# Performance work log

Measured on AMD Instinct MI355X. Metric: run time of the kernel, lower is better.

## Reference

```python
import jax, jax.numpy as jnp
import numpy as np

ALPHA_U = 1.0 / 10.0   # dt/tauu
ALPHA_V = 1.0 / 150.0  # dt/tauv
M = 10.0

def setup_inputs() -> dict:
    key = jax.random.key(0)
    ks = jax.random.split(key, 6)
    B, D_in, H = 8192, 1024, 2048
    stdv = 1.0 / np.sqrt(H)
    return {
        "x": jax.random.normal(ks[0], (B, D_in), dtype=jnp.float32),
        "u": jax.random.normal(ks[1], (B, H), dtype=jnp.float32),
        "v": jax.random.normal(ks[2], (B, H), dtype=jnp.float32),
        "win": jax.random.uniform(ks[3], (H, D_in), dtype=jnp.float32, minval=-stdv, maxval=stdv),
        "wr": jax.random.uniform(ks[4], (H, H), dtype=jnp.float32, minval=-stdv, maxval=stdv),
        "bias": jax.random.uniform(ks[5], (H,), dtype=jnp.float32, minval=-stdv, maxval=stdv),
    }

def reference(x, u, v, win, wr, bias):
    # v update: leaky blend toward m*u, then relu
    v_new = jax.nn.relu((1.0 - ALPHA_V) * v + (ALPHA_V * M) * u)
    # u update: leaky blend with input + recurrent drive minus adapted v
    drive = jnp.einsum('bi,hi->bh', x, win) + jnp.einsum('bk,hk->bh', u, wr) + bias - v_new
    u_new = jax.nn.relu((1.0 - ALPHA_U) * u + ALPHA_U * drive)
    return (u_new, v_new)
```

## Files before the change

kernel.cpp:

```cpp
#include <hip/hip_runtime.h>
#include <hip/hip_bf16.h>
#include <stdint.h>

#define B_DIM 8192
#define D_IN  1024
#define H_DIM 2048
#define K_DIM (D_IN + H_DIM)

#define CV_CONST  (1.0f - 1.0f/150.0f)
#define CUV_CONST (10.0f/150.0f)
#define CU_CONST  0.9f
#define AU_CONST  0.1f

typedef __attribute__((ext_vector_type(8))) short short8;
typedef __attribute__((ext_vector_type(4))) float floatx4;

__device__ __forceinline__ unsigned short f2bf(float f) {
    union { float f; unsigned u; } x; x.f = f;
    unsigned r = x.u + 0x7fffu + ((x.u >> 16) & 1u);
    return (unsigned short)(r >> 16);
}

#define N4_X   ((B_DIM * D_IN)  / 4)
#define N4_U   ((B_DIM * H_DIM) / 4)
#define N4_WIN ((H_DIM * D_IN)  / 4)
#define N4_WR  ((H_DIM * H_DIM) / 4)
#define N4_TOT (N4_X + N4_U + N4_WIN + N4_WR)

__global__ __launch_bounds__(256)
void pack_all(const float4* __restrict__ x, const float4* __restrict__ u,
              const float4* __restrict__ win, const float4* __restrict__ wr,
              unsigned short* __restrict__ Abf, unsigned short* __restrict__ Wbf) {
    int i = blockIdx.x * 256 + threadIdx.x;
    const float4* src; unsigned short* dst; int shift, mask, coloff;
    if (i < N4_X)                    { src = x;   dst = Abf; shift = 10; mask = 1023; coloff = 0;    }
    else if (i < N4_X + N4_U)        { i -= N4_X; src = u;   dst = Abf; shift = 11; mask = 2047; coloff = D_IN; }
    else if (i < N4_X + N4_U + N4_WIN){ i -= N4_X + N4_U; src = win; dst = Wbf; shift = 10; mask = 1023; coloff = 0; }
    else                             { i -= N4_X + N4_U + N4_WIN; src = wr; dst = Wbf; shift = 11; mask = 2047; coloff = D_IN; }
    int idx = i << 2;
    int r = idx >> shift;
    int c = idx & mask;
    float4 f = src[i];
    ushort4 o;
    o.x = f2bf(f.x); o.y = f2bf(f.y); o.z = f2bf(f.z); o.w = f2bf(f.w);
    *(ushort4*)(dst + (size_t)r * K_DIM + coloff + c) = o;
}

#define GLOAD_LDS16(gp, lp)                                                          \
    __builtin_amdgcn_global_load_lds(                                                \
        (const __attribute__((address_space(1))) unsigned int*)(gp),                 \
        (__attribute__((address_space(3))) unsigned int*)(lp), 16, 0, 0)

#define VMCNT(n)  asm volatile("s_waitcnt vmcnt(" #n ")" ::: "memory")
#define LGKM0     asm volatile("s_waitcnt lgkmcnt(0)" ::: "memory")
#define SCHEDB    __builtin_amdgcn_sched_barrier(0)
#define BAR       __builtin_amdgcn_s_barrier()
#define PRIO1     __builtin_amdgcn_s_setprio(1)
#define PRIO0     __builtin_amdgcn_s_setprio(0)

#define NT (K_DIM / 64)

#define ALO 0
#define BLO 16384
#define BHI 32768
#define AHI 49152

#define ES_STRIDE 68
#define ES_REGION (16 * ES_STRIDE)

__global__ __launch_bounds__(512, 2)
void gemm_fused(const unsigned short* __restrict__ A,
                const unsigned short* __restrict__ Wc,
                const float* __restrict__ u_in,
                const float* __restrict__ v_in,
                const float* __restrict__ bias,
                float* __restrict__ out)
{
    __shared__ __align__(16) unsigned char smem[131072];

    const int tid  = threadIdx.x;
    const int wave = tid >> 6;
    const int lane = tid & 63;
    const int wrh  = wave >> 2;
    const int wc   = wave & 3;

    const int bid   = blockIdx.x;
    const int wid   = ((bid & 7) << 5) | (bid >> 3);
    const int tileM = (wid >> 3) << 8;
    const int tileN = (wid & 7)  << 8;

    const int frow = lane & 15;
    const int g    = lane >> 4;

    const unsigned short* Ag = A  + (size_t)(tileM + (wave >> 1) * 16 + frow) * K_DIM
                                  + (wave & 1) * 32 + g * 8;
    const unsigned short* Bg = Wc + (size_t)(tileN + (wave >> 2) * 64 + ((wave >> 1) & 1) * 16 + frow) * K_DIM
                                  + (wave & 1) * 32 + g * 8;
    const size_t R128 = (size_t)128 * K_DIM;
    const size_t R64  = (size_t) 64 * K_DIM;
    const size_t R32  = (size_t) 32 * K_DIM;

    const int w1024 = wave << 10;

    const int aRd = (wrh << 13) + (lane << 4);
    const int bRd = (wc  << 12) + (lane << 4);

    GLOAD_LDS16(Ag,               smem + ALO + w1024);
    GLOAD_LDS16(Ag + R128,        smem + ALO + 8192 + w1024);
    GLOAD_LDS16(Bg,               smem + BLO + w1024);
    GLOAD_LDS16(Bg + R128,        smem + BLO + 8192 + w1024);
    GLOAD_LDS16(Bg + R32,         smem + BHI + w1024);
    GLOAD_LDS16(Bg + R32 + R128,  smem + BHI + 8192 + w1024);
    GLOAD_LDS16(Ag + R64,         smem + AHI + w1024);
    GLOAD_LDS16(Ag + R64 + R128,  smem + AHI + 8192 + w1024);

    floatx4 acc[8][4] = {};
    short8 Alo[4][2], Ahi[4][2], Bl[2][2], Bh[2][2];

#define RD_A(cb, unit, i2s) (*(const short8*)(smem + (cb) + (unit) + aRd + (i2s) * 1024))
#define RD_B(cb, unit, j2s) (*(const short8*)(smem + (cb) + (unit) + bRd + (j2s) * 1024))

#pragma unroll 2
    for (int t = 0; t < NT - 1; ++t) {
        const int cb = (t & 1) << 16;
        const int nb = cb ^ 65536;
        const size_t kk = (size_t)(t + 1) * 64;

        GLOAD_LDS16(Ag + kk,              smem + nb + ALO + w1024);
        GLOAD_LDS16(Ag + kk + R128,       smem + nb + ALO + 8192 + w1024);
        GLOAD_LDS16(Bg + kk,              smem + nb + BLO + w1024);
        GLOAD_LDS16(Bg + kk + R128,       smem + nb + BLO + 8192 + w1024);
        GLOAD_LDS16(Bg + kk + R32,        smem + nb + BHI + w1024);
        GLOAD_LDS16(Bg + kk + R32 + R128, smem + nb + BHI + 8192 + w1024);
        GLOAD_LDS16(Ag + kk + R64,        smem + nb + AHI + w1024);
        GLOAD_LDS16(Ag + kk + R64 + R128, smem + nb + AHI + 8192 + w1024);

        VMCNT(8);
        BAR;
        SCHEDB;

#pragma unroll
        for (int i = 0; i < 4; ++i) { Alo[i][0] = RD_A(cb, ALO, i*2); Alo[i][1] = RD_A(cb, ALO, i*2+1); }
#pragma unroll
        for (int j = 0; j < 2; ++j) { Bl[j][0] = RD_B(cb, BLO, j*2); Bl[j][1] = RD_B(cb, BLO, j*2+1); }
#pragma unroll
        for (int j = 0; j < 2; ++j) { Bh[j][0] = RD_B(cb, BHI, j*2); Bh[j][1] = RD_B(cb, BHI, j*2+1); }
#pragma unroll
        for (int i = 0; i < 4; ++i) { Ahi[i][0] = RD_A(cb, AHI, i*2); Ahi[i][1] = RD_A(cb, AHI, i*2+1); }

        PRIO1;
#pragma unroll
        for (int i = 0; i < 4; ++i)
#pragma unroll
            for (int j = 0; j < 2; ++j) {
                acc[i][j] = __builtin_amdgcn_mfma_f32_16x16x32_bf16(Alo[i][0], Bl[j][0], acc[i][j], 0, 0, 0);
                acc[i][j] = __builtin_amdgcn_mfma_f32_16x16x32_bf16(Alo[i][1], Bl[j][1], acc[i][j], 0, 0, 0);
            }
#pragma unroll
        for (int i = 0; i < 4; ++i)
#pragma unroll
            for (int j = 0; j < 2; ++j) {
                acc[i][2+j] = __builtin_amdgcn_mfma_f32_16x16x32_bf16(Alo[i][0], Bh[j][0], acc[i][2+j], 0, 0, 0);
                acc[i][2+j] = __builtin_amdgcn_mfma_f32_16x16x32_bf16(Alo[i][1], Bh[j][1], acc[i][2+j], 0, 0, 0);
            }
#pragma unroll
        for (int i = 0; i < 4; ++i)
#pragma unroll
            for (int j = 0; j < 2; ++j) {
                acc[4+i][2+j] = __builtin_amdgcn_mfma_f32_16x16x32_bf16(Ahi[i][0], Bh[j][0], acc[4+i][2+j], 0, 0, 0);
                acc[4+i][2+j] = __builtin_amdgcn_mfma_f32_16x16x32_bf16(Ahi[i][1], Bh[j][1], acc[4+i][2+j], 0, 0, 0);
            }
#pragma unroll
        for (int i = 0; i < 4; ++i)
#pragma unroll
            for (int j = 0; j < 2; ++j) {
                acc[4+i][j] = __builtin_amdgcn_mfma_f32_16x16x32_bf16(Ahi[i][0], Bl[j][0], acc[4+i][j], 0, 0, 0);
                acc[4+i][j] = __builtin_amdgcn_mfma_f32_16x16x32_bf16(Ahi[i][1], Bl[j][1], acc[4+i][j], 0, 0, 0);
            }
        PRIO0;

        LGKM0;
        BAR;
    }

    {
        const int cb = ((NT - 1) & 1) << 16;
        VMCNT(0);
        BAR;
        SCHEDB;
#pragma unroll
        for (int i = 0; i < 4; ++i) { Alo[i][0] = RD_A(cb, ALO, i*2); Alo[i][1] = RD_A(cb, ALO, i*2+1); }
#pragma unroll
        for (int j = 0; j < 2; ++j) { Bl[j][0] = RD_B(cb, BLO, j*2); Bl[j][1] = RD_B(cb, BLO, j*2+1); }
#pragma unroll
        for (int j = 0; j < 2; ++j) { Bh[j][0] = RD_B(cb, BHI, j*2); Bh[j][1] = RD_B(cb, BHI, j*2+1); }
#pragma unroll
        for (int i = 0; i < 4; ++i) { Ahi[i][0] = RD_A(cb, AHI, i*2); Ahi[i][1] = RD_A(cb, AHI, i*2+1); }

        PRIO1;
#pragma unroll
        for (int i = 0; i < 4; ++i)
#pragma unroll
            for (int j = 0; j < 2; ++j) {
                acc[i][j]     = __builtin_amdgcn_mfma_f32_16x16x32_bf16(Alo[i][0], Bl[j][0], acc[i][j],     0, 0, 0);
                acc[i][j]     = __builtin_amdgcn_mfma_f32_16x16x32_bf16(Alo[i][1], Bl[j][1], acc[i][j],     0, 0, 0);
                acc[i][2+j]   = __builtin_amdgcn_mfma_f32_16x16x32_bf16(Alo[i][0], Bh[j][0], acc[i][2+j],   0, 0, 0);
                acc[i][2+j]   = __builtin_amdgcn_mfma_f32_16x16x32_bf16(Alo[i][1], Bh[j][1], acc[i][2+j],   0, 0, 0);
                acc[4+i][2+j] = __builtin_amdgcn_mfma_f32_16x16x32_bf16(Ahi[i][0], Bh[j][0], acc[4+i][2+j], 0, 0, 0);
                acc[4+i][2+j] = __builtin_amdgcn_mfma_f32_16x16x32_bf16(Ahi[i][1], Bh[j][1], acc[4+i][2+j], 0, 0, 0);
                acc[4+i][j]   = __builtin_amdgcn_mfma_f32_16x16x32_bf16(Ahi[i][0], Bl[j][0], acc[4+i][j],   0, 0, 0);
                acc[4+i][j]   = __builtin_amdgcn_mfma_f32_16x16x32_bf16(Ahi[i][1], Bl[j][1], acc[4+i][j],   0, 0, 0);
            }
        PRIO0;
    }

    __syncthreads();

    float* Esf = (float*)smem;
    const int q    = lane >> 4;
    const int c16  = lane & 15;
    const int colg = tileN + wc * 64 + c16 * 4;
    const float4 b4 = *(const float4*)&bias[colg];
    const size_t outV = (size_t)B_DIM * H_DIM;

#pragma unroll
    for (int i = 0; i < 8; ++i) {
        float* Es = Esf + (wave * 2 + (i & 1)) * ES_REGION;
#pragma unroll
        for (int j = 0; j < 4; ++j)
#pragma unroll
            for (int r = 0; r < 4; ++r)
                Es[(q * 4 + r) * ES_STRIDE + j * 16 + c16] = acc[i][j][r];
#pragma unroll
        for (int rg = 0; rg < 4; rg++) {
            const int rloc = rg * 4 + q;
            const float4 a4 = *(const float4*)&Es[rloc * ES_STRIDE + c16 * 4];
            const size_t idx = (size_t)(tileM + wrh * 128 + i * 16 + rloc) * H_DIM + colg;
            const float4 u4 = *(const float4*)&u_in[idx];
            const float4 v4 = *(const float4*)&v_in[idx];
            float4 vn, un;
            vn.x = fmaxf(CV_CONST * v4.x + CUV_CONST * u4.x, 0.0f);
            vn.y = fmaxf(CV_CONST * v4.y + CUV_CONST * u4.y, 0.0f);
            vn.z = fmaxf(CV_CONST * v4.z + CUV_CONST * u4.z, 0.0f);
            vn.w = fmaxf(CV_CONST * v4.w + CUV_CONST * u4.w, 0.0f);
            un.x = fmaxf(CU_CONST * u4.x + AU_CONST * (a4.x + b4.x - vn.x), 0.0f);
            un.y = fmaxf(CU_CONST * u4.y + AU_CONST * (a4.y + b4.y - vn.y), 0.0f);
            un.z = fmaxf(CU_CONST * u4.z + AU_CONST * (a4.z + b4.z - vn.z), 0.0f);
            un.w = fmaxf(CU_CONST * u4.w + AU_CONST * (a4.w + b4.w - vn.w), 0.0f);
            *(float4*)&out[idx]        = un;
            *(float4*)&out[outV + idx] = vn;
        }
    }
}

extern "C" void kernel_launch(void* const* d_in, const int* in_sizes, int n_in,
                              void* d_out, int out_size, void* d_ws, size_t ws_size,
                              hipStream_t stream) {
    const float* x    = (const float*)d_in[0];
    const float* u    = (const float*)d_in[1];
    const float* v    = (const float*)d_in[2];
    const float* win  = (const float*)d_in[3];
    const float* wr   = (const float*)d_in[4];
    const float* bias = (const float*)d_in[5];
    float* out = (float*)d_out;

    unsigned short* Abf = (unsigned short*)d_ws;
    unsigned short* Wbf = Abf + (size_t)B_DIM * K_DIM;

    pack_all<<<N4_TOT / 256, 256, 0, stream>>>(
        (const float4*)x, (const float4*)u, (const float4*)win, (const float4*)wr,
        Abf, Wbf);

    gemm_fused<<<256, 512, 0, stream>>>(Abf, Wbf, u, v, bias, out);
}
```

Before: 389.3 us.

## Load B operand directly from global into registers and split main loop into phases

Stops staging the weight (B) tile through shared memory: each wave loads its own B fragments straight from global memory into double-buffered registers, while only the A tile still goes through LDS via direct global-to-LDS loads. The K loop is restructured into four MFMA phases with staggered A loads (lo/hi halves issued at different points) and explicit vmcnt/barrier placement. This cuts LDS traffic and LDS reads for B and frees shared-memory capacity. In exchange it uses more registers, duplicates B global loads across the waves of a block, adds more barriers, and depends on hand-tuned vmcnt counts being correct.

```diff
diff --git a/kernel.cpp b/kernel.cpp
--- a/kernel.cpp
+++ b/kernel.cpp
@@ -53,6 +53,7 @@
 
 #define VMCNT(n)  asm volatile("s_waitcnt vmcnt(" #n ")" ::: "memory")
 #define LGKM0     asm volatile("s_waitcnt lgkmcnt(0)" ::: "memory")
+#define CPIN      asm volatile("" ::: "memory")
 #define SCHEDB    __builtin_amdgcn_sched_barrier(0)
 #define BAR       __builtin_amdgcn_s_barrier()
 #define PRIO1     __builtin_amdgcn_s_setprio(1)
@@ -61,8 +62,6 @@
 #define NT (K_DIM / 64)
 
 #define ALO 0
-#define BLO 16384
-#define BHI 32768
 #define AHI 49152
 
 #define ES_STRIDE 68
@@ -94,122 +93,141 @@
 
     const unsigned short* Ag = A  + (size_t)(tileM + (wave >> 1) * 16 + frow) * K_DIM
                                   + (wave & 1) * 32 + g * 8;
-    const unsigned short* Bg = Wc + (size_t)(tileN + (wave >> 2) * 64 + ((wave >> 1) & 1) * 16 + frow) * K_DIM
-                                  + (wave & 1) * 32 + g * 8;
     const size_t R128 = (size_t)128 * K_DIM;
     const size_t R64  = (size_t) 64 * K_DIM;
-    const size_t R32  = (size_t) 32 * K_DIM;
+
+    const unsigned short* Br = Wc + (size_t)(tileN + wc * 64 + frow) * K_DIM + g * 8;
 
     const int w1024 = wave << 10;
 
     const int aRd = (wrh << 13) + (lane << 4);
-    const int bRd = (wc  << 12) + (lane << 4);
-
-    GLOAD_LDS16(Ag,               smem + ALO + w1024);
-    GLOAD_LDS16(Ag + R128,        smem + ALO + 8192 + w1024);
-    GLOAD_LDS16(Bg,               smem + BLO + w1024);
-    GLOAD_LDS16(Bg + R128,        smem + BLO + 8192 + w1024);
-    GLOAD_LDS16(Bg + R32,         smem + BHI + w1024);
-    GLOAD_LDS16(Bg + R32 + R128,  smem + BHI + 8192 + w1024);
-    GLOAD_LDS16(Ag + R64,         smem + AHI + w1024);
-    GLOAD_LDS16(Ag + R64 + R128,  smem + AHI + 8192 + w1024);
 
     floatx4 acc[8][4] = {};
-    short8 Alo[4][2], Ahi[4][2], Bl[2][2], Bh[2][2];
+    short8 Ar[4][2];
+    short8 Bb0[8], Bb1[8];
 
 #define RD_A(cb, unit, i2s) (*(const short8*)(smem + (cb) + (unit) + aRd + (i2s) * 1024))
-#define RD_B(cb, unit, j2s) (*(const short8*)(smem + (cb) + (unit) + bRd + (j2s) * 1024))
-
-#pragma unroll 2
-    for (int t = 0; t < NT - 1; ++t) {
-        const int cb = (t & 1) << 16;
-        const int nb = cb ^ 65536;
-        const size_t kk = (size_t)(t + 1) * 64;
-
-        GLOAD_LDS16(Ag + kk,              smem + nb + ALO + w1024);
-        GLOAD_LDS16(Ag + kk + R128,       smem + nb + ALO + 8192 + w1024);
-        GLOAD_LDS16(Bg + kk,              smem + nb + BLO + w1024);
-        GLOAD_LDS16(Bg + kk + R128,       smem + nb + BLO + 8192 + w1024);
-        GLOAD_LDS16(Bg + kk + R32,        smem + nb + BHI + w1024);
-        GLOAD_LDS16(Bg + kk + R32 + R128, smem + nb + BHI + 8192 + w1024);
-        GLOAD_LDS16(Ag + kk + R64,        smem + nb + AHI + w1024);
-        GLOAD_LDS16(Ag + kk + R64 + R128, smem + nb + AHI + 8192 + w1024);
-
-        VMCNT(8);
-        BAR;
-        SCHEDB;
-
-#pragma unroll
-        for (int i = 0; i < 4; ++i) { Alo[i][0] = RD_A(cb, ALO, i*2); Alo[i][1] = RD_A(cb, ALO, i*2+1); }
-#pragma unroll
-        for (int j = 0; j < 2; ++j) { Bl[j][0] = RD_B(cb, BLO, j*2); Bl[j][1] = RD_B(cb, BLO, j*2+1); }
-#pragma unroll
-        for (int j = 0; j < 2; ++j) { Bh[j][0] = RD_B(cb, BHI, j*2); Bh[j][1] = RD_B(cb, BHI, j*2+1); }
-#pragma unroll
-        for (int i = 0; i < 4; ++i) { Ahi[i][0] = RD_A(cb, AHI, i*2); Ahi[i][1] = RD_A(cb, AHI, i*2+1); }
-
+
+    GLOAD_LDS16(Ag,        smem + ALO + w1024);
+    GLOAD_LDS16(Ag + R128, smem + ALO + 8192 + w1024);
+    CPIN;
+#pragma unroll
+    for (int j = 0; j < 4; ++j) {
+        Bb0[j*2+0] = *(const short8*)(Br + (size_t)j * 16 * K_DIM);
+        Bb0[j*2+1] = *(const short8*)(Br + (size_t)j * 16 * K_DIM + 32);
+    }
+    CPIN;
+    GLOAD_LDS16(Ag + R64,        smem + AHI + w1024);
+    GLOAD_LDS16(Ag + R64 + R128, smem + AHI + 8192 + w1024);
+    VMCNT(10);
+    BAR; SCHEDB;
+
+#define TILE_BODY(T, CB, NB, BCUR, BNXT)                                             \
+    {                                                                                \
+        const size_t kk = (size_t)((T) + 1) * 64;                                    \
+                   \
+        GLOAD_LDS16(Ag + kk,        smem + (NB) + ALO + w1024);                      \
+        GLOAD_LDS16(Ag + kk + R128, smem + (NB) + ALO + 8192 + w1024);               \
+        _Pragma("unroll")                                                            \
+        for (int i = 0; i < 4; ++i) {                                                \
+            Ar[i][0] = RD_A(CB, ALO, i*2); Ar[i][1] = RD_A(CB, ALO, i*2+1);          \
+        }                                                                            \
+        VMCNT(4); BAR; LGKM0; SCHEDB;                                                \
+        PRIO1;                                                                       \
+        _Pragma("unroll")                                                            \
+        for (int i = 0; i < 4; ++i)                                                  \
+            _Pragma("unroll")                                                        \
+            for (int j = 0; j < 2; ++j) {                                            \
+                acc[i][j] = __builtin_amdgcn_mfma_f32_16x16x32_bf16(Ar[i][0], BCUR[j*2+0], acc[i][j], 0, 0, 0); \
+                acc[i][j] = __builtin_amdgcn_mfma_f32_16x16x32_bf16(Ar[i][1], BCUR[j*2+1], acc[i][j], 0, 0, 0); \
+            }                                                                        \
+        PRIO0; SCHEDB; BAR;                                                          \
+                                         \
+        _Pragma("unroll")                                                            \
+        for (int j = 0; j < 4; ++j) {                                                \
+            BNXT[j*2+0] = *(const short8*)(Br + (size_t)j * 16 * K_DIM + kk);        \
+            BNXT[j*2+1] = *(const short8*)(Br + (size_t)j * 16 * K_DIM + kk + 32);   \
+        }                                                                            \
+        CPIN;                                                                        \
+        PRIO1;                                                                       \
+        _Pragma("unroll")                                                            \
+        for (int i = 0; i < 4; ++i)                                                  \
+            _Pragma("unroll")                                                        \
+            for (int j = 0; j < 2; ++j) {                                            \
+                acc[i][2+j] = __builtin_amdgcn_mfma_f32_16x16x32_bf16(Ar[i][0], BCUR[4+j*2+0], acc[i][2+j], 0, 0, 0); \
+                acc[i][2+j] = __builtin_amdgcn_mfma_f32_16x16x32_bf16(Ar[i][1], BCUR[4+j*2+1], acc[i][2+j], 0, 0, 0); \
+            }                                                                        \
+        PRIO0; SCHEDB; BAR;                                                          \
+                         \
+        GLOAD_LDS16(Ag + kk + R64,        smem + (NB) + AHI + w1024);                \
+        GLOAD_LDS16(Ag + kk + R64 + R128, smem + (NB) + AHI + 8192 + w1024);         \
+        VMCNT(12); BAR; SCHEDB;                                                      \
+        _Pragma("unroll")                                                            \
+        for (int i = 0; i < 4; ++i) {                                                \
+            Ar[i][0] = RD_A(CB, AHI, i*2); Ar[i][1] = RD_A(CB, AHI, i*2+1);          \
+        }                                                                            \
+        LGKM0; SCHEDB;                                                               \
+        PRIO1;                                                                       \
+        _Pragma("unroll")                                                            \
+        for (int i = 0; i < 4; ++i)                                                  \
+            _Pragma("unroll")                                                        \
+            for (int j = 0; j < 2; ++j) {                                            \
+                acc[4+i][2+j] = __builtin_amdgcn_mfma_f32_16x16x32_bf16(Ar[i][0], BCUR[4+j*2+0], acc[4+i][2+j], 0, 0, 0); \
+                acc[4+i][2+j] = __builtin_amdgcn_mfma_f32_16x16x32_bf16(Ar[i][1], BCUR[4+j*2+1], acc[4+i][2+j], 0, 0, 0); \
+            }                                                                        \
+        PRIO0; SCHEDB; BAR;                                                          \
+                  \
+        PRIO1;                                                                       \
+        _Pragma("unroll")                                                            \
+        for (int i = 0; i < 4; ++i)                                                  \
+            _Pragma("unroll")                                                        \
+            for (int j = 0; j < 2; ++j) {                                            \
+                acc[4+i][j] = __builtin_amdgcn_mfma_f32_16x16x32_bf16(Ar[i][0], BCUR[j*2+0], acc[4+i][j], 0, 0, 0); \
+                acc[4+i][j] = __builtin_amdgcn_mfma_f32_16x16x32_bf16(Ar[i][1], BCUR[j*2+1], acc[4+i][j], 0, 0, 0); \
+            }                                                                        \
+        PRIO0; SCHEDB;                                                               \
+        VMCNT(10); LGKM0; BAR;                                                       \
+    }
+
+    for (int tp = 0; tp < 23; ++tp) {
+        const int t0 = tp * 2;
+        TILE_BODY(t0,     0,     65536, Bb0, Bb1)
+        TILE_BODY(t0 + 1, 65536, 0,     Bb1, Bb0)
+    }
+    TILE_BODY(46, 0, 65536, Bb0, Bb1)
+
+    {
+#pragma unroll
+        for (int i = 0; i < 4; ++i) {
+            Ar[i][0] = RD_A(65536, ALO, i*2); Ar[i][1] = RD_A(65536, ALO, i*2+1);
+        }
+        VMCNT(2); LGKM0; SCHEDB;
         PRIO1;
 #pragma unroll
         for (int i = 0; i < 4; ++i)
 #pragma unroll
             for (int j = 0; j < 2; ++j) {
-                acc[i][j] = __builtin_amdgcn_mfma_f32_16x16x32_bf16(Alo[i][0], Bl[j][0], acc[i][j], 0, 0, 0);
-                acc[i][j] = __builtin_amdgcn_mfma_f32_16x16x32_bf16(Alo[i][1], Bl[j][1], acc[i][j], 0, 0, 0);
+                acc[i][j]   = __builtin_amdgcn_mfma_f32_16x16x32_bf16(Ar[i][0], Bb1[j*2+0], acc[i][j],   0, 0, 0);
+                acc[i][j]   = __builtin_amdgcn_mfma_f32_16x16x32_bf16(Ar[i][1], Bb1[j*2+1], acc[i][j],   0, 0, 0);
+                acc[i][2+j] = __builtin_amdgcn_mfma_f32_16x16x32_bf16(Ar[i][0], Bb1[4+j*2+0], acc[i][2+j], 0, 0, 0);
+                acc[i][2+j] = __builtin_amdgcn_mfma_f32_16x16x32_bf16(Ar[i][1], Bb1[4+j*2+1], acc[i][2+j], 0, 0, 0);
             }
+        PRIO0; SCHEDB;
+        VMCNT(0); BAR; SCHEDB;
+#pragma unroll
+        for (int i = 0; i < 4; ++i) {
+            Ar[i][0] = RD_A(65536, AHI, i*2); Ar[i][1] = RD_A(65536, AHI, i*2+1);
+        }
+        LGKM0; SCHEDB;
+        PRIO1;
 #pragma unroll
         for (int i = 0; i < 4; ++i)
 #pragma unroll
             for (int j = 0; j < 2; ++j) {
-                acc[i][2+j] = __builtin_amdgcn_mfma_f32_16x16x32_bf16(Alo[i][0], Bh[j][0], acc[i][2+j], 0, 0, 0);
-                acc[i][2+j] = __builtin_amdgcn_mfma_f32_16x16x32_bf16(Alo[i][1], Bh[j][1], acc[i][2+j], 0, 0, 0);
-            }
-#pragma unroll
-        for (int i = 0; i < 4; ++i)
-#pragma unroll
-            for (int j = 0; j < 2; ++j) {
-                acc[4+i][2+j] = __builtin_amdgcn_mfma_f32_16x16x32_bf16(Ahi[i][0], Bh[j][0], acc[4+i][2+j], 0, 0, 0);
-                acc[4+i][2+j] = __builtin_amdgcn_mfma_f32_16x16x32_bf16(Ahi[i][1], Bh[j][1], acc[4+i][2+j], 0, 0, 0);
-            }
-#pragma unroll
-        for (int i = 0; i < 4; ++i)
-#pragma unroll
-            for (int j = 0; j < 2; ++j) {
-                acc[4+i][j] = __builtin_amdgcn_mfma_f32_16x16x32_bf16(Ahi[i][0], Bl[j][0], acc[4+i][j], 0, 0, 0);
-                acc[4+i][j] = __builtin_amdgcn_mfma_f32_16x16x32_bf16(Ahi[i][1], Bl[j][1], acc[4+i][j], 0, 0, 0);
-            }
-        PRIO0;
-
-        LGKM0;
-        BAR;
-    }
-
-    {
-        const int cb = ((NT - 1) & 1) << 16;
-        VMCNT(0);
-        BAR;
-        SCHEDB;
-#pragma unroll
-        for (int i = 0; i < 4; ++i) { Alo[i][0] = RD_A(cb, ALO, i*2); Alo[i][1] = RD_A(cb, ALO, i*2+1); }
-#pragma unroll
-        for (int j = 0; j < 2; ++j) { Bl[j][0] = RD_B(cb, BLO, j*2); Bl[j][1] = RD_B(cb, BLO, j*2+1); }
-#pragma unroll
-        for (int j = 0; j < 2; ++j) { Bh[j][0] = RD_B(cb, BHI, j*2); Bh[j][1] = RD_B(cb, BHI, j*2+1); }
-#pragma unroll
-        for (int i = 0; i < 4; ++i) { Ahi[i][0] = RD_A(cb, AHI, i*2); Ahi[i][1] = RD_A(cb, AHI, i*2+1); }
-
-        PRIO1;
-#pragma unroll
-        for (int i = 0; i < 4; ++i)
-#pragma unroll
-            for (int j = 0; j < 2; ++j) {
-                acc[i][j]     = __builtin_amdgcn_mfma_f32_16x16x32_bf16(Alo[i][0], Bl[j][0], acc[i][j],     0, 0, 0);
-                acc[i][j]     = __builtin_amdgcn_mfma_f32_16x16x32_bf16(Alo[i][1], Bl[j][1], acc[i][j],     0, 0, 0);
-                acc[i][2+j]   = __builtin_amdgcn_mfma_f32_16x16x32_bf16(Alo[i][0], Bh[j][0], acc[i][2+j],   0, 0, 0);
-                acc[i][2+j]   = __builtin_amdgcn_mfma_f32_16x16x32_bf16(Alo[i][1], Bh[j][1], acc[i][2+j],   0, 0, 0);
-                acc[4+i][2+j] = __builtin_amdgcn_mfma_f32_16x16x32_bf16(Ahi[i][0], Bh[j][0], acc[4+i][2+j], 0, 0, 0);
-                acc[4+i][2+j] = __builtin_amdgcn_mfma_f32_16x16x32_bf16(Ahi[i][1], Bh[j][1], acc[4+i][2+j], 0, 0, 0);
-                acc[4+i][j]   = __builtin_amdgcn_mfma_f32_16x16x32_bf16(Ahi[i][0], Bl[j][0], acc[4+i][j],   0, 0, 0);
-                acc[4+i][j]   = __builtin_amdgcn_mfma_f32_16x16x32_bf16(Ahi[i][1], Bl[j][1], acc[4+i][j],   0, 0, 0);
+                acc[4+i][2+j] = __builtin_amdgcn_mfma_f32_16x16x32_bf16(Ar[i][0], Bb1[4+j*2+0], acc[4+i][2+j], 0, 0, 0);
+                acc[4+i][2+j] = __builtin_amdgcn_mfma_f32_16x16x32_bf16(Ar[i][1], Bb1[4+j*2+1], acc[4+i][2+j], 0, 0, 0);
+                acc[4+i][j]   = __builtin_amdgcn_mfma_f32_16x16x32_bf16(Ar[i][0], Bb1[j*2+0], acc[4+i][j],   0, 0, 0);
+                acc[4+i][j]   = __builtin_amdgcn_mfma_f32_16x16x32_bf16(Ar[i][1], Bb1[j*2+1], acc[4+i][j],   0, 0, 0);
             }
         PRIO0;
     }
```

After: 430.7 us. 10.6% more time.

## Split K-tile into four quadrant phases with staggered loads and prefetch epilogue u/v

Applied to the files above, without the earlier changes.

Each K iteration is restructured into four MFMA quadrant phases, each issuing the next tile's loads for the LDS region it just freed and waiting on a finer vmcnt. This interleaves global loads with compute more evenly and lets the A fragments share one register set. In the first 16 tiles it also issues dummy 4-byte global-to-LDS loads of u and v into a scratch LDS region, to warm the cache for the epilogue. The cost is more barriers per tile, slightly more LDS, and one extra outstanding load per tile in the vmcnt accounting.

```diff
diff --git a/kernel.cpp b/kernel.cpp
--- a/kernel.cpp
+++ b/kernel.cpp
@@ -51,6 +51,11 @@
         (const __attribute__((address_space(1))) unsigned int*)(gp),                 \
         (__attribute__((address_space(3))) unsigned int*)(lp), 16, 0, 0)
 
+#define GLOAD_LDS4(gp, lp)                                                           \
+    __builtin_amdgcn_global_load_lds(                                                \
+        (const __attribute__((address_space(1))) unsigned int*)(gp),                 \
+        (__attribute__((address_space(3))) unsigned int*)(lp), 4, 0, 0)
+
 #define VMCNT(n)  asm volatile("s_waitcnt vmcnt(" #n ")" ::: "memory")
 #define LGKM0     asm volatile("s_waitcnt lgkmcnt(0)" ::: "memory")
 #define SCHEDB    __builtin_amdgcn_sched_barrier(0)
@@ -64,6 +69,7 @@
 #define BLO 16384
 #define BHI 32768
 #define AHI 49152
+#define DUMP 131072
 
 #define ES_STRIDE 68
 #define ES_REGION (16 * ES_STRIDE)
@@ -76,7 +82,7 @@
                 const float* __restrict__ bias,
                 float* __restrict__ out)
 {
-    __shared__ __align__(16) unsigned char smem[131072];
+    __shared__ __align__(16) unsigned char smem[133120];
 
     const int tid  = threadIdx.x;
     const int wave = tid >> 6;
@@ -104,6 +110,12 @@
 
     const int aRd = (wrh << 13) + (lane << 4);
     const int bRd = (wc  << 12) + (lane << 4);
+
+    const size_t trow = (size_t)(tileM + wave * 4 + (lane >> 4)) * H_DIM
+                      + tileN + (lane & 15) * 16;
+    const float* tpu = u_in + trow;
+    const float* tpv = v_in + trow;
+    unsigned char* dump = smem + DUMP + (wave << 8);
 
     GLOAD_LDS16(Ag,               smem + ALO + w1024);
     GLOAD_LDS16(Ag + R128,        smem + ALO + 8192 + w1024);
@@ -114,102 +126,142 @@
     GLOAD_LDS16(Ag + R64,         smem + AHI + w1024);
     GLOAD_LDS16(Ag + R64 + R128,  smem + AHI + 8192 + w1024);
 
+    VMCNT(4);
+    BAR;
+    LGKM0;
+
     floatx4 acc[8][4] = {};
-    short8 Alo[4][2], Ahi[4][2], Bl[2][2], Bh[2][2];
+    short8 Ar[4][2], Bl[2][2], Bh[2][2];
 
 #define RD_A(cb, unit, i2s) (*(const short8*)(smem + (cb) + (unit) + aRd + (i2s) * 1024))
 #define RD_B(cb, unit, j2s) (*(const short8*)(smem + (cb) + (unit) + bRd + (j2s) * 1024))
 
-#pragma unroll 2
-    for (int t = 0; t < NT - 1; ++t) {
-        const int cb = (t & 1) << 16;
-        const int nb = cb ^ 65536;
-        const size_t kk = (size_t)(t + 1) * 64;
-
-        GLOAD_LDS16(Ag + kk,              smem + nb + ALO + w1024);
-        GLOAD_LDS16(Ag + kk + R128,       smem + nb + ALO + 8192 + w1024);
-        GLOAD_LDS16(Bg + kk,              smem + nb + BLO + w1024);
-        GLOAD_LDS16(Bg + kk + R128,       smem + nb + BLO + 8192 + w1024);
-        GLOAD_LDS16(Bg + kk + R32,        smem + nb + BHI + w1024);
-        GLOAD_LDS16(Bg + kk + R32 + R128, smem + nb + BHI + 8192 + w1024);
-        GLOAD_LDS16(Ag + kk + R64,        smem + nb + AHI + w1024);
-        GLOAD_LDS16(Ag + kk + R64 + R128, smem + nb + AHI + 8192 + w1024);
-
-        VMCNT(8);
-        BAR;
-        SCHEDB;
-
-#pragma unroll
-        for (int i = 0; i < 4; ++i) { Alo[i][0] = RD_A(cb, ALO, i*2); Alo[i][1] = RD_A(cb, ALO, i*2+1); }
-#pragma unroll
-        for (int j = 0; j < 2; ++j) { Bl[j][0] = RD_B(cb, BLO, j*2); Bl[j][1] = RD_B(cb, BLO, j*2+1); }
-#pragma unroll
-        for (int j = 0; j < 2; ++j) { Bh[j][0] = RD_B(cb, BHI, j*2); Bh[j][1] = RD_B(cb, BHI, j*2+1); }
-#pragma unroll
-        for (int i = 0; i < 4; ++i) { Ahi[i][0] = RD_A(cb, AHI, i*2); Ahi[i][1] = RD_A(cb, AHI, i*2+1); }
-
-        PRIO1;
-#pragma unroll
-        for (int i = 0; i < 4; ++i)
-#pragma unroll
-            for (int j = 0; j < 2; ++j) {
-                acc[i][j] = __builtin_amdgcn_mfma_f32_16x16x32_bf16(Alo[i][0], Bl[j][0], acc[i][j], 0, 0, 0);
-                acc[i][j] = __builtin_amdgcn_mfma_f32_16x16x32_bf16(Alo[i][1], Bl[j][1], acc[i][j], 0, 0, 0);
-            }
-#pragma unroll
-        for (int i = 0; i < 4; ++i)
-#pragma unroll
-            for (int j = 0; j < 2; ++j) {
-                acc[i][2+j] = __builtin_amdgcn_mfma_f32_16x16x32_bf16(Alo[i][0], Bh[j][0], acc[i][2+j], 0, 0, 0);
-                acc[i][2+j] = __builtin_amdgcn_mfma_f32_16x16x32_bf16(Alo[i][1], Bh[j][1], acc[i][2+j], 0, 0, 0);
-            }
-#pragma unroll
-        for (int i = 0; i < 4; ++i)
-#pragma unroll
-            for (int j = 0; j < 2; ++j) {
-                acc[4+i][2+j] = __builtin_amdgcn_mfma_f32_16x16x32_bf16(Ahi[i][0], Bh[j][0], acc[4+i][2+j], 0, 0, 0);
-                acc[4+i][2+j] = __builtin_amdgcn_mfma_f32_16x16x32_bf16(Ahi[i][1], Bh[j][1], acc[4+i][2+j], 0, 0, 0);
-            }
-#pragma unroll
-        for (int i = 0; i < 4; ++i)
-#pragma unroll
-            for (int j = 0; j < 2; ++j) {
-                acc[4+i][j] = __builtin_amdgcn_mfma_f32_16x16x32_bf16(Ahi[i][0], Bl[j][0], acc[4+i][j], 0, 0, 0);
-                acc[4+i][j] = __builtin_amdgcn_mfma_f32_16x16x32_bf16(Ahi[i][1], Bl[j][1], acc[4+i][j], 0, 0, 0);
-            }
-        PRIO0;
-
-        LGKM0;
-        BAR;
+#define K_TILE(T, TCH, NA, NB)                                                       \
+    {                                                                                \
+        const int cb = ((T) & 1) << 16;                                              \
+        const int nb = cb ^ 65536;                                                   \
+        const size_t kk = (size_t)((T) + 1) * 64;                                    \
+             \
+             \
+        TCH                                                                          \
+        GLOAD_LDS16(Ag + kk,        smem + nb + ALO + w1024);                        \
+        GLOAD_LDS16(Ag + kk + R128, smem + nb + ALO + 8192 + w1024);                 \
+        _Pragma("unroll")                                                            \
+        for (int i = 0; i < 4; ++i) { Ar[i][0] = RD_A(cb, ALO, i*2); Ar[i][1] = RD_A(cb, ALO, i*2+1); } \
+        _Pragma("unroll")                                                            \
+        for (int j = 0; j < 2; ++j) { Bl[j][0] = RD_B(cb, BLO, j*2); Bl[j][1] = RD_B(cb, BLO, j*2+1); } \
+        VMCNT(NA); BAR; LGKM0; SCHEDB;                                               \
+        PRIO1;                                                                       \
+        _Pragma("unroll")                                                            \
+        for (int i = 0; i < 4; ++i)                                                  \
+            _Pragma("unroll")                                                        \
+            for (int j = 0; j < 2; ++j) {                                            \
+                acc[i][j] = __builtin_amdgcn_mfma_f32_16x16x32_bf16(Ar[i][0], Bl[j][0], acc[i][j], 0, 0, 0); \
+                acc[i][j] = __builtin_amdgcn_mfma_f32_16x16x32_bf16(Ar[i][1], Bl[j][1], acc[i][j], 0, 0, 0); \
+            }                                                                        \
+        PRIO0; SCHEDB; BAR;                                                          \
+                         \
+        GLOAD_LDS16(Bg + kk,        smem + nb + BLO + w1024);                        \
+        GLOAD_LDS16(Bg + kk + R128, smem + nb + BLO + 8192 + w1024);                 \
+        _Pragma("unroll")                                                            \
+        for (int j = 0; j < 2; ++j) { Bh[j][0] = RD_B(cb, BHI, j*2); Bh[j][1] = RD_B(cb, BHI, j*2+1); } \
+        VMCNT(NB); BAR; LGKM0; SCHEDB;                                               \
+        PRIO1;                                                                       \
+        _Pragma("unroll")                                                            \
+        for (int i = 0; i < 4; ++i)                                                  \
+            _Pragma("unroll")                                                        \
+            for (int j = 0; j < 2; ++j) {                                            \
+                acc[i][2+j] = __builtin_amdgcn_mfma_f32_16x16x32_bf16(Ar[i][0], Bh[j][0], acc[i][2+j], 0, 0, 0); \
+                acc[i][2+j] = __builtin_amdgcn_mfma_f32_16x16x32_bf16(Ar[i][1], Bh[j][1], acc[i][2+j], 0, 0, 0); \
+            }                                                                        \
+        PRIO0; SCHEDB; BAR;                                                          \
+            \
+        GLOAD_LDS16(Bg + kk + R32,        smem + nb + BHI + w1024);                  \
+        GLOAD_LDS16(Bg + kk + R32 + R128, smem + nb + BHI + 8192 + w1024);           \
+        _Pragma("unroll")                                                            \
+        for (int i = 0; i < 4; ++i) { Ar[i][0] = RD_A(cb, AHI, i*2); Ar[i][1] = RD_A(cb, AHI, i*2+1); } \
+        BAR; LGKM0; SCHEDB;                                                          \
+        PRIO1;                                                                       \
+        _Pragma("unroll")                                                            \
+        for (int i = 0; i < 4; ++i)                                                  \
+            _Pragma("unroll")                                                        \
+            for (int j = 0; j < 2; ++j) {                                            \
+                acc[4+i][2+j] = __builtin_amdgcn_mfma_f32_16x16x32_bf16(Ar[i][0], Bh[j][0], acc[4+i][2+j], 0, 0, 0); \
+                acc[4+i][2+j] = __builtin_amdgcn_mfma_f32_16x16x32_bf16(Ar[i][1], Bh[j][1], acc[4+i][2+j], 0, 0, 0); \
+            }                                                                        \
+        PRIO0; SCHEDB; BAR;                                                          \
+            \
+        GLOAD_LDS16(Ag + kk + R64,        smem + nb + AHI + w1024);                  \
+        GLOAD_LDS16(Ag + kk + R64 + R128, smem + nb + AHI + 8192 + w1024);           \
+        VMCNT(4); BAR; LGKM0; SCHEDB;                                                \
+        PRIO1;                                                                       \
+        _Pragma("unroll")                                                            \
+        for (int i = 0; i < 4; ++i)                                                  \
+            _Pragma("unroll")                                                        \
+            for (int j = 0; j < 2; ++j) {                                            \
+                acc[4+i][j] = __builtin_amdgcn_mfma_f32_16x16x32_bf16(Ar[i][0], Bl[j][0], acc[4+i][j], 0, 0, 0); \
+                acc[4+i][j] = __builtin_amdgcn_mfma_f32_16x16x32_bf16(Ar[i][1], Bl[j][1], acc[4+i][j], 0, 0, 0); \
+            }                                                                        \
+        PRIO0; SCHEDB; BAR;                                                          \
     }
+
+#define TOUCH_U { GLOAD_LDS4(tpu, dump); tpu += 32 * (size_t)H_DIM; }
+#define TOUCH_V { GLOAD_LDS4(tpv, dump); tpv += 32 * (size_t)H_DIM; }
+#define TOUCH_NONE
+
+    for (int t = 0; t < 8; ++t)   K_TILE(t, TOUCH_U, 5, 5)
+    for (int t = 8; t < 16; ++t)  K_TILE(t, TOUCH_V, 5, 5)
+    for (int t = 16; t < NT - 1; ++t) K_TILE(t, TOUCH_NONE, 4, 4)
 
     {
         const int cb = ((NT - 1) & 1) << 16;
+#pragma unroll
+        for (int i = 0; i < 4; ++i) { Ar[i][0] = RD_A(cb, ALO, i*2); Ar[i][1] = RD_A(cb, ALO, i*2+1); }
+#pragma unroll
+        for (int j = 0; j < 2; ++j) { Bl[j][0] = RD_B(cb, BLO, j*2); Bl[j][1] = RD_B(cb, BLO, j*2+1); }
+        VMCNT(2);
+        BAR; LGKM0; SCHEDB;
+        PRIO1;
+#pragma unroll
+        for (int i = 0; i < 4; ++i)
+#pragma unroll
+            for (int j = 0; j < 2; ++j) {
+                acc[i][j] = __builtin_amdgcn_mfma_f32_16x16x32_bf16(Ar[i][0], Bl[j][0], acc[i][j], 0, 0, 0);
+                acc[i][j] = __builtin_amdgcn_mfma_f32_16x16x32_bf16(Ar[i][1], Bl[j][1], acc[i][j], 0, 0, 0);
+            }
+        PRIO0; SCHEDB; BAR;
+#pragma unroll
+        for (int j = 0; j < 2; ++j) { Bh[j][0] = RD_B(cb, BHI, j*2); Bh[j][1] = RD_B(cb, BHI, j*2+1); }
         VMCNT(0);
-        BAR;
-        SCHEDB;
-#pragma unroll
-        for (int i = 0; i < 4; ++i) { Alo[i][0] = RD_A(cb, ALO, i*2); Alo[i][1] = RD_A(cb, ALO, i*2+1); }
-#pragma unroll
-        for (int j = 0; j < 2; ++j) { Bl[j][0] = RD_B(cb, BLO, j*2); Bl[j][1] = RD_B(cb, BLO, j*2+1); }
-#pragma unroll
-        for (int j = 0; j < 2; ++j) { Bh[j][0] = RD_B(cb, BHI, j*2); Bh[j][1] = RD_B(cb, BHI, j*2+1); }
-#pragma unroll
-        for (int i = 0; i < 4; ++i) { Ahi[i][0] = RD_A(cb, AHI, i*2); Ahi[i][1] = RD_A(cb, AHI, i*2+1); }
-
+        BAR; LGKM0; SCHEDB;
         PRIO1;
 #pragma unroll
         for (int i = 0; i < 4; ++i)
 #pragma unroll
             for (int j = 0; j < 2; ++j) {
-                acc[i][j]     = __builtin_amdgcn_mfma_f32_16x16x32_bf16(Alo[i][0], Bl[j][0], acc[i][j],     0, 0, 0);
-                acc[i][j]     = __builtin_amdgcn_mfma_f32_16x16x32_bf16(Alo[i][1], Bl[j][1], acc[i][j],     0, 0, 0);
-                acc[i][2+j]   = __builtin_amdgcn_mfma_f32_16x16x32_bf16(Alo[i][0], Bh[j][0], acc[i][2+j],   0, 0, 0);
-                acc[i][2+j]   = __builtin_amdgcn_mfma_f32_16x16x32_bf16(Alo[i][1], Bh[j][1], acc[i][2+j],   0, 0, 0);
-                acc[4+i][2+j] = __builtin_amdgcn_mfma_f32_16x16x32_bf16(Ahi[i][0], Bh[j][0], acc[4+i][2+j], 0, 0, 0);
-                acc[4+i][2+j] = __builtin_amdgcn_mfma_f32_16x16x32_bf16(Ahi[i][1], Bh[j][1], acc[4+i][2+j], 0, 0, 0);
-                acc[4+i][j]   = __builtin_amdgcn_mfma_f32_16x16x32_bf16(Ahi[i][0], Bl[j][0], acc[4+i][j],   0, 0, 0);
-                acc[4+i][j]   = __builtin_amdgcn_mfma_f32_16x16x32_bf16(Ahi[i][1], Bl[j][1], acc[4+i][j],   0, 0, 0);
+                acc[i][2+j] = __builtin_amdgcn_mfma_f32_16x16x32_bf16(Ar[i][0], Bh[j][0], acc[i][2+j], 0, 0, 0);
+                acc[i][2+j] = __builtin_amdgcn_mfma_f32_16x16x32_bf16(Ar[i][1], Bh[j][1], acc[i][2+j], 0, 0, 0);
+            }
+        PRIO0; SCHEDB; BAR;
+#pragma unroll
+        for (int i = 0; i < 4; ++i) { Ar[i][0] = RD_A(cb, AHI, i*2); Ar[i][1] = RD_A(cb, AHI, i*2+1); }
+        BAR; LGKM0; SCHEDB;
+        PRIO1;
+#pragma unroll
+        for (int i = 0; i < 4; ++i)
+#pragma unroll
+            for (int j = 0; j < 2; ++j) {
+                acc[4+i][2+j] = __builtin_amdgcn_mfma_f32_16x16x32_bf16(Ar[i][0], Bh[j][0], acc[4+i][2+j], 0, 0, 0);
+                acc[4+i][2+j] = __builtin_amdgcn_mfma_f32_16x16x32_bf16(Ar[i][1], Bh[j][1], acc[4+i][2+j], 0, 0, 0);
+            }
+        PRIO0; SCHEDB; BAR;
+        PRIO1;
+#pragma unroll
+        for (int i = 0; i < 4; ++i)
+#pragma unroll
+            for (int j = 0; j < 2; ++j) {
+                acc[4+i][j] = __builtin_amdgcn_mfma_f32_16x16x32_bf16(Ar[i][0], Bl[j][0], acc[4+i][j], 0, 0, 0);
+                acc[4+i][j] = __builtin_amdgcn_mfma_f32_16x16x32_bf16(Ar[i][1], Bl[j][1], acc[4+i][j], 0, 0, 0);
             }
         PRIO0;
     }
```

After: 385.6 us. No clear change (-1.0%).
